# Kernel optimization log

Measured on AMD Instinct MI355X. Metric: run time of the kernel, lower is better.

The kernel has to match this reference:

```python
import jax, jax.numpy as jnp
import numpy as np

N = 100000      # nodes
E = 1600000     # edges (avg degree 16)
D = 128         # in = hid = out dim


def setup_inputs() -> dict:
    key = jax.random.key(0)
    ks = jax.random.split(key, 7)
    x = jax.random.normal(ks[0], (N, D), dtype=jnp.float32)
    src = jax.random.randint(ks[1], (E,), 0, N, dtype=jnp.int32)
    dst = jax.random.randint(ks[2], (E,), 0, N, dtype=jnp.int32)
    s = 1.0 / np.sqrt(2 * D)  # torch Linear default init bound
    W0 = jax.random.uniform(ks[3], (D, 2 * D), jnp.float32, -s, s)
    b0 = jax.random.uniform(ks[4], (D,), jnp.float32, -s, s)
    W1 = jax.random.uniform(ks[5], (D, 2 * D), jnp.float32, -s, s)
    b1 = jax.random.uniform(ks[6], (D,), jnp.float32, -s, s)
    return {"x": x, "src": src, "dst": dst, "W0": W0, "b0": b0, "W1": W1, "b1": b1}


def graph_conv_left(x, src, dst):
    """DGL GraphConv(norm='left', weight=False, bias=False):
    h_v = sum_{(u->v) in E} x_u / max(outdeg(u), 1)."""
    n = x.shape[0]
    deg = jax.ops.segment_sum(jnp.ones_like(src, dtype=x.dtype), src, num_segments=n)
    deg = jnp.maximum(deg, 1.0)
    msgs = (x / deg[:, None])[src]          # [E, D] gather of normalized src feats
    return jax.ops.segment_sum(msgs, dst, num_segments=n)  # [N, D] scatter-add


def reference(x, src, dst, W0, b0, W1, b1):
    # layer 0: concat(self, agg) -> linear -> relu
    h = jnp.concatenate([x, graph_conv_left(x, src, dst)], axis=1)  # [N, 2D]
    h = jax.nn.relu(h @ W0.T + b0)                                  # [N, D]
    # layer 1 (output): concat -> linear (no relu)
    out = jnp.concatenate([h, graph_conv_left(h, src, dst)], axis=1) @ W1.T + b1
    return out
```

## Files before the change

kernel.cpp:

```cpp
#include <hip/hip_runtime.h>
#include <hip/hip_fp16.h>

#define DIM 128
#define CAP 64
#define BW_LOG 8
#define BW_NODES 256
#define CHUNK_P 4096
#define KCELL 40
#define MAXCHUNK 512

typedef _Float16 f16x8 __attribute__((ext_vector_type(8)));
typedef float f32x4 __attribute__((ext_vector_type(4)));
typedef unsigned int uint;

__global__ __launch_bounds__(512) void k_front(const int* __restrict__ src,
                                               const int* __restrict__ dst,
                                               uint* __restrict__ dbuf,
                                               uint* __restrict__ sbuf,
                                               uint* __restrict__ cntD,
                                               uint* __restrict__ cntS,
                                               const float* __restrict__ W0,
                                               const float* __restrict__ W1,
                                               const float* __restrict__ x,
                                               _Float16* __restrict__ Wr0,
                                               _Float16* __restrict__ Wr1,
                                               __half* __restrict__ fh,
                                               int E, int NB, int nchunk, int nquadX) {
    if ((int)blockIdx.x >= nchunk) {
        int i = ((int)blockIdx.x - nchunk) * 512 + threadIdx.x;
        if (i < 8192) {
            const float* W = (i < 4096) ? W0 : W1;
            _Float16* Wr  = (i < 4096) ? Wr0 : Wr1;
            int j = i & 4095;
            int f = j >> 6;
            int ln = j & 63;
            int ks = f >> 3, t = f & 7;
            int col = t * 16 + (ln & 15);
            int k0 = ks * 32 + (ln >> 4) * 8;
            const float* wsrc = W + (size_t)col * 256 + k0;
            float4 va = *(const float4*)wsrc;
            float4 vb = *(const float4*)(wsrc + 4);
            __half2* o = (__half2*)(Wr + ((size_t)f * 64 + ln) * 8);
            o[0] = __floats2half2_rn(va.x, va.y);
            o[1] = __floats2half2_rn(va.z, va.w);
            o[2] = __floats2half2_rn(vb.x, vb.y);
            o[3] = __floats2half2_rn(vb.z, vb.w);
            return;
        }
        int q = i - 8192;
        if (q >= nquadX) return;
        float4 v = ((const float4*)x)[q];
        __half2* o = (__half2*)fh;
        o[q * 2]     = __floats2half2_rn(v.x, v.y);
        o[q * 2 + 1] = __floats2half2_rn(v.z, v.w);
        return;
    }
    extern __shared__ uint smem[];
    uint* rb    = smem;
    uint* cells = smem + NB;
    int blk = blockIdx.x;
    int e0 = blk * CHUNK_P;

    int4 sv[2], dv[2];
    bool ok[2];
#pragma unroll
    for (int q = 0; q < 2; ++q) {
        int i4 = (e0 >> 2) + q * 512 + (int)threadIdx.x;
        int e = i4 << 2;
        ok[q] = (e < E);
        if (ok[q]) {
            sv[q] = ((const int4*)src)[i4];
            dv[q] = ((const int4*)dst)[i4];
        }
    }

    const int KQ = KCELL / 4;
    int nq = NB * KQ;

    for (int i = threadIdx.x; i < NB; i += 512) rb[i] = 0;
    __syncthreads();
#pragma unroll
    for (int q = 0; q < 2; ++q) {
        if (!ok[q]) continue;
        int ds[4] = {dv[q].x, dv[q].y, dv[q].z, dv[q].w};
        int ss[4] = {sv[q].x, sv[q].y, sv[q].z, sv[q].w};
#pragma unroll
        for (int k = 0; k < 4; ++k) {
            uint d = (uint)ds[k];
            uint bd = d >> BW_LOG;
            uint r = atomicAdd(&rb[bd], 1);
            if (r < KCELL)
                cells[bd * KCELL + r] = ((d & (BW_NODES - 1)) << 17) | (uint)ss[k];
        }
    }
    __syncthreads();
    for (int u = threadIdx.x; u < nq; u += 512) {
        int bucket = u / KQ;
        int s4 = u - bucket * KQ;
        ((uint4*)dbuf)[((size_t)bucket * nchunk + blk) * KQ + s4] = ((const uint4*)cells)[u];
    }
    for (int i = threadIdx.x; i < NB; i += 512) {
        uint c = rb[i];
        cntD[(uint)i * nchunk + blk] = c < KCELL ? c : KCELL;
    }
    __syncthreads();

    for (int i = threadIdx.x; i < NB; i += 512) rb[i] = 0;
    __syncthreads();
#pragma unroll
    for (int q = 0; q < 2; ++q) {
        if (!ok[q]) continue;
        int ss[4] = {sv[q].x, sv[q].y, sv[q].z, sv[q].w};
#pragma unroll
        for (int k = 0; k < 4; ++k) {
            uint s = (uint)ss[k];
            uint bs = s >> BW_LOG;
            uint r = atomicAdd(&rb[bs], 1);
            if (r < KCELL)
                cells[bs * KCELL + r] = s;
        }
    }
    __syncthreads();
    for (int u = threadIdx.x; u < nq; u += 512) {
        int bucket = u / KQ;
        int s4 = u - bucket * KQ;
        ((uint4*)sbuf)[((size_t)bucket * nchunk + blk) * KQ + s4] = ((const uint4*)cells)[u];
    }
    for (int i = threadIdx.x; i < NB; i += 512) {
        uint c = rb[i];
        cntS[(uint)i * nchunk + blk] = c < KCELL ? c : KCELL;
    }
}

__global__ __launch_bounds__(512) void k_build(const uint* __restrict__ dbuf,
                                               const uint* __restrict__ cntD,
                                               const uint* __restrict__ sbuf,
                                               const uint* __restrict__ cntS,
                                               int* __restrict__ edge_pad,
                                               int* __restrict__ cnt,
                                               float* __restrict__ invd,
                                               int N, int NB, int nchunk) {
    __shared__ uint mcell[MAXCHUNK];
    __shared__ uint cur[BW_NODES];
    __shared__ int  img[128 * CAP];
    int gid = blockIdx.x;
    if (gid < NB) {
        int b = gid;
        for (int c = threadIdx.x; c < nchunk; c += 512)
            mcell[c] = cntD[(uint)b * nchunk + c];
        uint base = (uint)b * nchunk * KCELL;
        int total = nchunk * KCELL;
        int node0 = b << BW_LOG;
        for (int g = 0; g < 2; ++g) {
            int l0 = g << 7;
            for (int i = threadIdx.x; i < 128; i += 512) cur[i] = 0;
            __syncthreads();
            uint v[4]; bool val[4];
            for (int sb = 0; sb < total; sb += 2048) {
#pragma unroll
                for (int q = 0; q < 4; ++q) {
                    int s = sb + q * 512 + (int)threadIdx.x;
                    val[q] = false;
                    if (s < total) {
                        int c = s / KCELL;
                        int j = s - c * KCELL;
                        if ((uint)j < mcell[c]) { val[q] = true; v[q] = dbuf[base + s]; }
                    }
                }
#pragma unroll
                for (int q = 0; q < 4; ++q) {
                    if (val[q]) {
                        uint local = v[q] >> 17;
                        if ((int)(local >> 7) == g) {
                            uint slot = atomicAdd(&cur[local - l0], 1);
                            if (slot < CAP)
                                img[(local - l0) * CAP + slot] = (int)(v[q] & 0x1FFFFu);
                        }
                    }
                }
            }
            __syncthreads();
            int4* gp = (int4*)&edge_pad[(size_t)(node0 + l0) * CAP];
            const int4* lp = (const int4*)img;
            for (int i = threadIdx.x; i < 128 * CAP / 4; i += 512) {
                int row = i >> 4;
                if (node0 + l0 + row < N) gp[i] = lp[i];
            }
            for (int i = threadIdx.x; i < 128; i += 512) {
                int node = node0 + l0 + i;
                if (node < N) cnt[node] = (int)(cur[i] < CAP ? cur[i] : CAP);
            }
            __syncthreads();
        }
    } else {
        int b = gid - NB;
        for (int c = threadIdx.x; c < nchunk; c += 512)
            mcell[c] = cntS[(uint)b * nchunk + c];
        for (int i = threadIdx.x; i < BW_NODES; i += 512) cur[i] = 0;
        __syncthreads();
        uint base = (uint)b * nchunk * KCELL;
        int total = nchunk * KCELL;
        uint v[4]; bool val[4];
        for (int sb = 0; sb < total; sb += 2048) {
#pragma unroll
            for (int q = 0; q < 4; ++q) {
                int s = sb + q * 512 + (int)threadIdx.x;
                val[q] = false;
                if (s < total) {
                    int c = s / KCELL;
                    int j = s - c * KCELL;
                    if ((uint)j < mcell[c]) { val[q] = true; v[q] = sbuf[base + s]; }
                }
            }
#pragma unroll
            for (int q = 0; q < 4; ++q)
                if (val[q]) atomicAdd(&cur[v[q] & (BW_NODES - 1)], 1);
        }
        __syncthreads();
        int node0 = b << BW_LOG;
        for (int i = threadIdx.x; i < BW_NODES; i += 512) {
            int node = node0 + i;
            if (node < N) {
                uint d = cur[i];
                invd[node] = 1.0f / (float)(d > 1u ? d : 1u);
            }
        }
    }
}

template <bool RELU, bool OUT16>
__global__ __launch_bounds__(256) void k_fused(const __half* __restrict__ feat,
                                               const float* __restrict__ invd,
                                               const int* __restrict__ edge_pad,
                                               const int* __restrict__ cnt_arr,
                                               const _Float16* __restrict__ Wr,
                                               const float* __restrict__ bias,
                                               float* __restrict__ out32,
                                               _Float16* __restrict__ out16,
                                               int n_rows) {
    __shared__ _Float16 agg[64 * 136];
    int tid  = threadIdx.x;
    int wave = tid >> 6;
    int lane = tid & 63;
    int quad = lane >> 4;
    int lq   = lane & 15;
    int rowbase = blockIdx.x * 64 + wave * 16;

    for (int nn = 0; nn < 16; ++nn) {
        int v = rowbase + nn;
        if (v >= n_rows) break;
        int cnt = cnt_arr[v];
        if (cnt > CAP) cnt = CAP;
        int u_lane = 0;
        float w_lane = 0.f;
        if (lane < cnt) {
            u_lane = edge_pad[(size_t)v * CAP + lane];
            w_lane = invd[u_lane];
        }
        float acc[8] = {0.f, 0.f, 0.f, 0.f, 0.f, 0.f, 0.f, 0.f};
        int cntUp = (cnt + 7) & ~7;
        for (int j = 0; j < cntUp; j += 8) {
            int   ua = __shfl(u_lane, j + quad);
            float wa = __shfl(w_lane, j + quad);
            int   ub = __shfl(u_lane, j + 4 + quad);
            float wb = __shfl(w_lane, j + 4 + quad);
            uint4 ra = *(const uint4*)&feat[(size_t)ua * 128 + lq * 8];
            uint4 rb = *(const uint4*)&feat[(size_t)ub * 128 + lq * 8];
            const __half2* pa = (const __half2*)&ra;
            const __half2* pb = (const __half2*)&rb;
#pragma unroll
            for (int i = 0; i < 4; ++i) {
                float2 fa = __half22float2(pa[i]);
                float2 fb = __half22float2(pb[i]);
                acc[2 * i]     = fmaf(fa.x, wa, acc[2 * i]);
                acc[2 * i + 1] = fmaf(fa.y, wa, acc[2 * i + 1]);
                acc[2 * i]     = fmaf(fb.x, wb, acc[2 * i]);
                acc[2 * i + 1] = fmaf(fb.y, wb, acc[2 * i + 1]);
            }
        }
#pragma unroll
        for (int off = 16; off <= 32; off <<= 1) {
#pragma unroll
            for (int i = 0; i < 8; ++i) acc[i] += __shfl_xor(acc[i], off);
        }
        if (quad == 0) {
            __half2 o[4];
#pragma unroll
            for (int i = 0; i < 4; ++i) o[i] = __floats2half2_rn(acc[2 * i], acc[2 * i + 1]);
            *(uint4*)&agg[(wave * 16 + nn) * 136 + lq * 8] = *(const uint4*)o;
        }
    }

    f32x4 acc[8] = {};
    int myrow = rowbase + lq;
    size_t ar = (size_t)(myrow < n_rows ? myrow : 0);
    const _Float16* fp = (const _Float16*)feat;
    int aggoff = (wave * 16 + lq) * 136 + quad * 8;
#pragma unroll
    for (int ks = 0; ks < 8; ++ks) {
        f16x8 a;
        if (ks < 4) a = *(const f16x8*)&fp[ar * 128 + ks * 32 + quad * 8];
        else        a = *(const f16x8*)&agg[aggoff + (ks - 4) * 32];
#pragma unroll
        for (int t = 0; t < 8; ++t) {
            f16x8 b = *(const f16x8*)&Wr[((size_t)((ks * 8 + t) * 64 + lane)) * 8];
            acc[t] = __builtin_amdgcn_mfma_f32_16x16x32_f16(a, b, acc[t], 0, 0, 0);
        }
    }
#pragma unroll
    for (int t = 0; t < 8; ++t) {
        int col = t * 16 + lq;
        float bv = bias[col];
#pragma unroll
        for (int r = 0; r < 4; ++r) {
            int row = rowbase + quad * 4 + r;
            if (row < n_rows) {
                float v = acc[t][r] + bv;
                if (RELU) v = fmaxf(v, 0.f);
                if (OUT16) out16[(size_t)row * 128 + col] = (_Float16)v;
                else       out32[(size_t)row * 128 + col] = v;
            }
        }
    }
}

extern "C" void kernel_launch(void* const* d_in, const int* in_sizes, int n_in,
                              void* d_out, int out_size, void* d_ws, size_t ws_size,
                              hipStream_t stream) {
    const float* x  = (const float*)d_in[0];
    const int*   src = (const int*)d_in[1];
    const int*   dst = (const int*)d_in[2];
    const float* W0 = (const float*)d_in[3];
    const float* b0 = (const float*)d_in[4];
    const float* W1 = (const float*)d_in[5];
    const float* b1 = (const float*)d_in[6];
    int N = in_sizes[0] / DIM;
    int E = in_sizes[1];
    float* out = (float*)d_out;
    int NB = (N + BW_NODES - 1) >> BW_LOG;
    int nchunk = (E + CHUNK_P - 1) / CHUNK_P;
    size_t ncell = (size_t)NB * nchunk;
    size_t cellWords = ncell * KCELL;

    char* p = (char*)d_ws;
    uint* cntDc = (uint*)p; p += (ncell * 4 + 63) & ~(size_t)63;
    uint* cntSc = (uint*)p; p += (ncell * 4 + 63) & ~(size_t)63;
    int*   edge_pad = (int*)p;   p += (size_t)N * CAP * 4;
    int*   cnt  = (int*)p;  p += ((size_t)N * 4 + 63) & ~(size_t)63;
    float* invd = (float*)p; p += ((size_t)N * 4 + 63) & ~(size_t)63;
    size_t featB = (size_t)N * DIM * 2;
    size_t cellB = cellWords * 4;
    size_t uniSz = cellB > featB ? cellB : featB;
    char*  uni = p; p += (uniSz + 63) & ~(size_t)63;
    uint*   dbuf = (uint*)uni;
    __half* fh   = (__half*)p; p += featB;
    char*  uni2 = p; p += (uniSz + 63) & ~(size_t)63;
    uint*   sbuf = (uint*)uni2;
    __half* hh   = (__half*)uni2;
    _Float16* Wr0 = (_Float16*)p; p += 64 * 64 * 8 * 2;
    _Float16* Wr1 = (_Float16*)p; p += 64 * 64 * 8 * 2;
    (void)ws_size; (void)n_in; (void)out_size;

    int nquadX = N * DIM / 4;
    int gP = (8192 + nquadX + 511) / 512;
    size_t shScatter = (size_t)(NB + NB * KCELL) * 4;
    k_front<<<nchunk + gP, 512, shScatter, stream>>>(src, dst, dbuf, sbuf, cntDc, cntSc,
                                                     W0, W1, x, Wr0, Wr1, fh,
                                                     E, NB, nchunk, nquadX);

    k_build<<<2 * NB, 512, 0, stream>>>(dbuf, cntDc, sbuf, cntSc,
                                        edge_pad, cnt, invd, N, NB, nchunk);

    int gF = (N + 63) / 64;

    k_fused<true, true><<<gF, 256, 0, stream>>>(fh, invd, edge_pad, cnt,
                                                Wr0, b0, nullptr, (_Float16*)hh, N);

    k_fused<false, false><<<gF, 256, 0, stream>>>(hh, invd, edge_pad, cnt,
                                                  Wr1, b1, out, nullptr, N);
}
```

Baseline: 348.3 us.

## Split fused gather+GEMM into separate gather and GEMM kernels

Replaces the fused kernel, in which each wave serially aggregated 16 nodes into shared memory before an MFMA GEMM, with two kernels. One is a gather kernel that assigns one wave per node, giving far more parallel waves to hide the latency of the random feature loads. The other is a GEMM kernel that processes 32 rows per wave and reuses each weight fragment across two MFMA tiles. The trade-off is that the aggregated features now make an extra round trip through global memory in fp16, plus two more kernel launches.

```diff
diff --git a/kernel.cpp b/kernel.cpp
--- a/kernel.cpp
+++ b/kernel.cpp
@@ -228,97 +228,111 @@
     }
 }
 
+__global__ __launch_bounds__(256) void k_gather(const __half* __restrict__ feat,
+                                                const float* __restrict__ invd,
+                                                const int* __restrict__ edge_pad,
+                                                const int* __restrict__ cnt_arr,
+                                                __half* __restrict__ agg, int n) {
+    int v = blockIdx.x * 4 + (threadIdx.x >> 6);
+    int lane = threadIdx.x & 63;
+    int quad = lane >> 4;
+    int lq   = lane & 15;
+    if (v >= n) return;
+    int cnt = cnt_arr[v];
+    if (cnt > CAP) cnt = CAP;
+
+    int u_lane = 0;
+    float w_lane = 0.f;
+    if (lane < cnt) {
+        u_lane = edge_pad[(size_t)v * CAP + lane];
+        w_lane = invd[u_lane];
+    }
+
+    float acc[8] = {0.f, 0.f, 0.f, 0.f, 0.f, 0.f, 0.f, 0.f};
+    int cntUp = (cnt + 7) & ~7;
+    for (int j = 0; j < cntUp; j += 8) {
+        int   ua = __shfl(u_lane, j + quad);
+        float wa = __shfl(w_lane, j + quad);
+        int   ub = __shfl(u_lane, j + 4 + quad);
+        float wb = __shfl(w_lane, j + 4 + quad);
+        uint4 ra = *(const uint4*)&feat[(size_t)ua * 128 + lq * 8];
+        uint4 rb = *(const uint4*)&feat[(size_t)ub * 128 + lq * 8];
+        const __half2* pa = (const __half2*)&ra;
+        const __half2* pb = (const __half2*)&rb;
+#pragma unroll
+        for (int i = 0; i < 4; ++i) {
+            float2 fa = __half22float2(pa[i]);
+            float2 fb = __half22float2(pb[i]);
+            acc[2 * i]     = fmaf(fa.x, wa, acc[2 * i]);
+            acc[2 * i + 1] = fmaf(fa.y, wa, acc[2 * i + 1]);
+            acc[2 * i]     = fmaf(fb.x, wb, acc[2 * i]);
+            acc[2 * i + 1] = fmaf(fb.y, wb, acc[2 * i + 1]);
+        }
+    }
+#pragma unroll
+    for (int off = 16; off <= 32; off <<= 1) {
+#pragma unroll
+        for (int i = 0; i < 8; ++i) acc[i] += __shfl_xor(acc[i], off);
+    }
+    if (quad == 0) {
+        __half2 o[4];
+#pragma unroll
+        for (int i = 0; i < 4; ++i) o[i] = __floats2half2_rn(acc[2 * i], acc[2 * i + 1]);
+        *(uint4*)&agg[(size_t)v * 128 + lq * 8] = *(const uint4*)o;
+    }
+}
+
 template <bool RELU, bool OUT16>
-__global__ __launch_bounds__(256) void k_fused(const __half* __restrict__ feat,
-                                               const float* __restrict__ invd,
-                                               const int* __restrict__ edge_pad,
-                                               const int* __restrict__ cnt_arr,
-                                               const _Float16* __restrict__ Wr,
-                                               const float* __restrict__ bias,
-                                               float* __restrict__ out32,
-                                               _Float16* __restrict__ out16,
-                                               int n_rows) {
-    __shared__ _Float16 agg[64 * 136];
+__global__ __launch_bounds__(256) void k_gemm_f16(const _Float16* __restrict__ A0,
+                                                  const _Float16* __restrict__ A1,
+                                                  const _Float16* __restrict__ Wr,
+                                                  const float* __restrict__ bias,
+                                                  float* __restrict__ out32,
+                                                  _Float16* __restrict__ out16,
+                                                  int n_rows) {
     int tid  = threadIdx.x;
     int wave = tid >> 6;
     int lane = tid & 63;
     int quad = lane >> 4;
-    int lq   = lane & 15;
-    int rowbase = blockIdx.x * 64 + wave * 16;
-
-    for (int nn = 0; nn < 16; ++nn) {
-        int v = rowbase + nn;
-        if (v >= n_rows) break;
-        int cnt = cnt_arr[v];
-        if (cnt > CAP) cnt = CAP;
-        int u_lane = 0;
-        float w_lane = 0.f;
-        if (lane < cnt) {
-            u_lane = edge_pad[(size_t)v * CAP + lane];
-            w_lane = invd[u_lane];
-        }
-        float acc[8] = {0.f, 0.f, 0.f, 0.f, 0.f, 0.f, 0.f, 0.f};
-        int cntUp = (cnt + 7) & ~7;
-        for (int j = 0; j < cntUp; j += 8) {
-            int   ua = __shfl(u_lane, j + quad);
-            float wa = __shfl(w_lane, j + quad);
-            int   ub = __shfl(u_lane, j + 4 + quad);
-            float wb = __shfl(w_lane, j + 4 + quad);
-            uint4 ra = *(const uint4*)&feat[(size_t)ua * 128 + lq * 8];
-            uint4 rb = *(const uint4*)&feat[(size_t)ub * 128 + lq * 8];
-            const __half2* pa = (const __half2*)&ra;
-            const __half2* pb = (const __half2*)&rb;
-#pragma unroll
-            for (int i = 0; i < 4; ++i) {
-                float2 fa = __half22float2(pa[i]);
-                float2 fb = __half22float2(pb[i]);
-                acc[2 * i]     = fmaf(fa.x, wa, acc[2 * i]);
-                acc[2 * i + 1] = fmaf(fa.y, wa, acc[2 * i + 1]);
-                acc[2 * i]     = fmaf(fb.x, wb, acc[2 * i]);
-                acc[2 * i + 1] = fmaf(fb.y, wb, acc[2 * i + 1]);
-            }
-        }
-#pragma unroll
-        for (int off = 16; off <= 32; off <<= 1) {
-#pragma unroll
-            for (int i = 0; i < 8; ++i) acc[i] += __shfl_xor(acc[i], off);
-        }
-        if (quad == 0) {
-            __half2 o[4];
-#pragma unroll
-            for (int i = 0; i < 4; ++i) o[i] = __floats2half2_rn(acc[2 * i], acc[2 * i + 1]);
-            *(uint4*)&agg[(wave * 16 + nn) * 136 + lq * 8] = *(const uint4*)o;
-        }
-    }
-
-    f32x4 acc[8] = {};
-    int myrow = rowbase + lq;
-    size_t ar = (size_t)(myrow < n_rows ? myrow : 0);
-    const _Float16* fp = (const _Float16*)feat;
-    int aggoff = (wave * 16 + lq) * 136 + quad * 8;
+    int l16  = lane & 15;
+    int m0 = blockIdx.x * 128 + wave * 32;
+
+    f32x4 acc[2][8] = {};
+
+    int ra = m0 + l16;
+    int rb = m0 + 16 + l16;
+    size_t r0 = (size_t)(ra < n_rows ? ra : 0);
+    size_t r1 = (size_t)(rb < n_rows ? rb : 0);
+
 #pragma unroll
     for (int ks = 0; ks < 8; ++ks) {
-        f16x8 a;
-        if (ks < 4) a = *(const f16x8*)&fp[ar * 128 + ks * 32 + quad * 8];
-        else        a = *(const f16x8*)&agg[aggoff + (ks - 4) * 32];
+        const _Float16* Ab = (ks < 4) ? A0 : A1;
+        int kk = (ks & 3) * 32 + quad * 8;
+        f16x8 a0 = *(const f16x8*)&Ab[r0 * 128 + kk];
+        f16x8 a1 = *(const f16x8*)&Ab[r1 * 128 + kk];
 #pragma unroll
         for (int t = 0; t < 8; ++t) {
             f16x8 b = *(const f16x8*)&Wr[((size_t)((ks * 8 + t) * 64 + lane)) * 8];
-            acc[t] = __builtin_amdgcn_mfma_f32_16x16x32_f16(a, b, acc[t], 0, 0, 0);
-        }
-    }
+            acc[0][t] = __builtin_amdgcn_mfma_f32_16x16x32_f16(a0, b, acc[0][t], 0, 0, 0);
+            acc[1][t] = __builtin_amdgcn_mfma_f32_16x16x32_f16(a1, b, acc[1][t], 0, 0, 0);
+        }
+    }
+
 #pragma unroll
     for (int t = 0; t < 8; ++t) {
-        int col = t * 16 + lq;
+        int col = t * 16 + l16;
         float bv = bias[col];
 #pragma unroll
-        for (int r = 0; r < 4; ++r) {
-            int row = rowbase + quad * 4 + r;
-            if (row < n_rows) {
-                float v = acc[t][r] + bv;
-                if (RELU) v = fmaxf(v, 0.f);
-                if (OUT16) out16[(size_t)row * 128 + col] = (_Float16)v;
-                else       out32[(size_t)row * 128 + col] = v;
+        for (int g = 0; g < 2; ++g) {
+#pragma unroll
+            for (int r = 0; r < 4; ++r) {
+                int row = m0 + g * 16 + quad * 4 + r;
+                if (row < n_rows) {
+                    float v = acc[g][t][r] + bv;
+                    if (RELU) v = fmaxf(v, 0.f);
+                    if (OUT16) out16[(size_t)row * 128 + col] = (_Float16)v;
+                    else       out32[(size_t)row * 128 + col] = v;
+                }
             }
         }
     }
@@ -353,12 +367,13 @@
     size_t uniSz = cellB > featB ? cellB : featB;
     char*  uni = p; p += (uniSz + 63) & ~(size_t)63;
     uint*   dbuf = (uint*)uni;
+    __half* aggh = (__half*)uni;
     __half* fh   = (__half*)p; p += featB;
     char*  uni2 = p; p += (uniSz + 63) & ~(size_t)63;
     uint*   sbuf = (uint*)uni2;
     __half* hh   = (__half*)uni2;
-    _Float16* Wr0 = (_Float16*)p; p += 64 * 64 * 8 * 2;
-    _Float16* Wr1 = (_Float16*)p; p += 64 * 64 * 8 * 2;
+    _Float16* Wr0 = (_Float16*)p; p += 64 * 64 * 8 * sizeof(_Float16);
+    _Float16* Wr1 = (_Float16*)p; p += 64 * 64 * 8 * sizeof(_Float16);
     (void)ws_size; (void)n_in; (void)out_size;
 
     int nquadX = N * DIM / 4;
@@ -371,11 +386,14 @@
     k_build<<<2 * NB, 512, 0, stream>>>(dbuf, cntDc, sbuf, cntSc,
                                         edge_pad, cnt, invd, N, NB, nchunk);
 
-    int gF = (N + 63) / 64;
-
-    k_fused<true, true><<<gF, 256, 0, stream>>>(fh, invd, edge_pad, cnt,
-                                                Wr0, b0, nullptr, (_Float16*)hh, N);
-
-    k_fused<false, false><<<gF, 256, 0, stream>>>(hh, invd, edge_pad, cnt,
-                                                  Wr1, b1, out, nullptr, N);
-}
+    int gG = (N + 3) / 4;
+    int gM = (N + 127) / 128;
+
+    k_gather<<<gG, 256, 0, stream>>>(fh, invd, edge_pad, cnt, aggh, N);
+    k_gemm_f16<true, true><<<gM, 256, 0, stream>>>((const _Float16*)fh, (const _Float16*)aggh,
+                                                   Wr0, b0, nullptr, (_Float16*)hh, N);
+
+    k_gather<<<gG, 256, 0, stream>>>(hh, invd, edge_pad, cnt, aggh, N);
+    k_gemm_f16<false, false><<<gM, 256, 0, stream>>>((const _Float16*)hh, (const _Float16*)aggh,
+                                                     Wr1, b1, out, nullptr, N);
+}
```

Result: faster. 340.3 us (-2.3%).
